# Optimization experiments

Hardware: AMD Instinct MI355X
Metric: run time of the kernel (lower is better)

Reference implementation:

```python
import jax, jax.numpy as jnp
import numpy as np

D_MODEL = 512
T_MAX = 200.0


def setup_inputs() -> dict:
    key = jax.random.key(0)
    k1, k2 = jax.random.split(key)
    B, L = 8, 2048
    event_type = jax.random.randint(k1, (B, L), 0, 2, dtype=jnp.int64 if jax.config.jax_enable_x64 else jnp.int32)
    event_time = jax.random.uniform(k2, (B, L), dtype=jnp.float32) * 200.0
    # learned params (num_types == 1 path)
    length_scale_param = jnp.asarray(1.0, dtype=jnp.float32)   # kernel.length_scale
    gate_params = jnp.asarray([0.1, 0.1], dtype=jnp.float32)   # sigmoid gate (l, s) pre-sigmoid
    return {"event_type": event_type, "event_time": event_time,
            "length_scale_param": length_scale_param, "gate_params": gate_params}


def reference(event_type, event_time, length_scale_param, gate_params):
    B, L = event_time.shape
    # temporal positional encoding: sin on even dims, cos on odd dims
    i = jnp.arange(D_MODEL)
    pos_vec = jnp.power(10000.0, 2.0 * i / D_MODEL).astype(event_time.dtype)
    te = event_time[:, :, None] / pos_vec                      # [B, L, d]
    embedding = jnp.where(i % 2 == 0, jnp.sin(te), jnp.cos(te))

    # pairwise time differences: xt[b,i,j] = t[b,i], xt_bar[b,i,j] = t[b,j]
    t_diff = event_time[:, :, None] - event_time[:, None, :]   # [B, L, L]
    d_abs = jnp.abs(t_diff)                                    # norm = 1

    # squared-exponential kernel (sigma = 1)
    ls = jax.nn.softplus(length_scale_param)
    kern = jnp.exp(-(d_abs ** 2) / (ls ** 2))

    # sigmoid gate: d = |diff / t_max|, gate = 1 + tanh((d - l) / s)
    l = jax.nn.sigmoid(gate_params[0])
    s = jax.nn.sigmoid(gate_params[1])
    gate = 1.0 + jnp.tanh((d_abs / T_MAX - l) / s)

    # causal mask: 1 on lower triangle incl. diagonal, 0 strictly above
    mask = jnp.tril(jnp.ones((L, L), dtype=event_time.dtype))
    scores = kern * gate * mask

    return scores, embedding, t_diff
```

## Files before the change

kernel.cpp:

```cpp
#include <hip/hip_runtime.h>

#define BATCH   8
#define LEN     2048
#define DMODEL  512
#define T_MAX   200.0f

__global__ __launch_bounds__(256) void scores_tdiff_kernel(
    const float* __restrict__ t,
    const float* __restrict__ ls_p,
    const float* __restrict__ gate_p,
    float* __restrict__ scores,
    float* __restrict__ tdiff)
{
    const int row = blockIdx.x;
    const int b   = row >> 11;
    const int i   = row & (LEN - 1);
    const int tid = threadIdx.x;
    const int c0  = tid * 4;
    const int c1  = 1024 + c0;

    const float ti = t[row];

    const float ls      = log1pf(__expf(ls_p[0]));
    const float inv_ls2 = 1.0f / (ls * ls);
    const float l = 1.0f / (1.0f + __expf(-gate_p[0]));
    const float s = 1.0f / (1.0f + __expf(-gate_p[1]));
    const float inv_s2 = 2.0f / s;
    const float invT   = 1.0f / T_MAX;

    const float* trow = t + b * LEN;
    float4 ta = *(const float4*)(trow + c0);
    float4 tb = *(const float4*)(trow + c1);
    float tj[8] = {ta.x, ta.y, ta.z, ta.w, tb.x, tb.y, tb.z, tb.w};
    int   col[8] = {c0, c0 + 1, c0 + 2, c0 + 3, c1, c1 + 1, c1 + 2, c1 + 3};

    float sc[8], td[8];
#pragma unroll
    for (int k = 0; k < 8; ++k) {
        float d  = ti - tj[k];
        float ad = fabsf(d);
        float kern = __expf(-ad * ad * inv_ls2);
        float u2 = (ad * invT - l) * inv_s2;
        float gate = __fdividef(2.0f, 1.0f + __expf(-u2));
        sc[k] = (col[k] <= i) ? kern * gate : 0.0f;
        td[k] = d;
    }

    size_t base = (size_t)row * LEN;
    *(float4*)(scores + base + c0) = make_float4(sc[0], sc[1], sc[2], sc[3]);
    *(float4*)(scores + base + c1) = make_float4(sc[4], sc[5], sc[6], sc[7]);
    *(float4*)(tdiff  + base + c0) = make_float4(td[0], td[1], td[2], td[3]);
    *(float4*)(tdiff  + base + c1) = make_float4(td[4], td[5], td[6], td[7]);
}

__global__ __launch_bounds__(256) void embed_kernel(
    const float* __restrict__ t,
    float* __restrict__ emb)
{
    const int tid = threadIdx.x;
    const int row = blockIdx.x * 2 + (tid >> 7);
    const int d0  = (tid & 127) * 4;

    const float tv = t[row];
    const float c = -9.210340371976184f * (2.0f / (float)DMODEL);

    float e[4];
#pragma unroll
    for (int k = 0; k < 4; k += 2) {
        int dim = d0 + k;
        float inv_pe = __expf(c * (float)dim);
        float inv_po = __expf(c * (float)(dim + 1));
        e[k]     = __sinf(tv * inv_pe);
        e[k + 1] = __cosf(tv * inv_po);
    }
    *(float4*)(emb + (size_t)row * DMODEL + d0) = make_float4(e[0], e[1], e[2], e[3]);
}

extern "C" void kernel_launch(void* const* d_in, const int* in_sizes, int n_in,
                              void* d_out, int out_size, void* d_ws, size_t ws_size,
                              hipStream_t stream) {
    const float* t      = (const float*)d_in[1];
    const float* ls_p   = (const float*)d_in[2];
    const float* gate_p = (const float*)d_in[3];

    float* out = (float*)d_out;
    const size_t n_scores = (size_t)BATCH * LEN * LEN;
    const size_t n_emb    = (size_t)BATCH * LEN * DMODEL;
    float* scores = out;
    float* emb    = out + n_scores;
    float* tdiff  = out + n_scores + n_emb;

    scores_tdiff_kernel<<<BATCH * LEN, 256, 0, stream>>>(t, ls_p, gate_p, scores, tdiff);
    embed_kernel<<<BATCH * LEN / 2, 256, 0, stream>>>(t, emb);
}
```

Baseline: 295.5 us.

## Fuse all outputs into one flat persistent streaming kernel with nontemporal stores

```diff
diff --git a/kernel.cpp b/kernel.cpp
--- a/kernel.cpp
+++ b/kernel.cpp
@@ -5,21 +5,25 @@
 #define DMODEL  512
 #define T_MAX   200.0f
 
-__global__ __launch_bounds__(256) void scores_tdiff_kernel(
+typedef float floatx4 __attribute__((ext_vector_type(4)));
+
+
+#define SC_CHUNKS   8388608u
+#define EMB_CHUNKS  2097152u
+#define TD_CHUNKS   8388608u
+#define EMB_BASE    SC_CHUNKS
+#define TD_BASE     (SC_CHUNKS + EMB_CHUNKS)
+#define NBLOCKS     2048
+#define ITERS       36
+
+__global__ __launch_bounds__(256) void fused_stream_kernel(
     const float* __restrict__ t,
     const float* __restrict__ ls_p,
     const float* __restrict__ gate_p,
-    float* __restrict__ scores,
-    float* __restrict__ tdiff)
+    float* __restrict__ out)
 {
-    const int row = blockIdx.x;
-    const int b   = row >> 11;
-    const int i   = row & (LEN - 1);
-    const int tid = threadIdx.x;
-    const int c0  = tid * 4;
-    const int c1  = 1024 + c0;
-
-    const float ti = t[row];
+    const unsigned tid  = threadIdx.x;
+    const unsigned base = blockIdx.x * (ITERS * 256u);
 
     const float ls      = log1pf(__expf(ls_p[0]));
     const float inv_ls2 = 1.0f / (ls * ls);
@@ -27,53 +31,61 @@
     const float s = 1.0f / (1.0f + __expf(-gate_p[1]));
     const float inv_s2 = 2.0f / s;
     const float invT   = 1.0f / T_MAX;
-
-    const float* trow = t + b * LEN;
-    float4 ta = *(const float4*)(trow + c0);
-    float4 tb = *(const float4*)(trow + c1);
-    float tj[8] = {ta.x, ta.y, ta.z, ta.w, tb.x, tb.y, tb.z, tb.w};
-    int   col[8] = {c0, c0 + 1, c0 + 2, c0 + 3, c1, c1 + 1, c1 + 2, c1 + 3};
-
-    float sc[8], td[8];
-#pragma unroll
-    for (int k = 0; k < 8; ++k) {
-        float d  = ti - tj[k];
-        float ad = fabsf(d);
-        float kern = __expf(-ad * ad * inv_ls2);
-        float u2 = (ad * invT - l) * inv_s2;
-        float gate = __fdividef(2.0f, 1.0f + __expf(-u2));
-        sc[k] = (col[k] <= i) ? kern * gate : 0.0f;
-        td[k] = d;
-    }
-
-    size_t base = (size_t)row * LEN;
-    *(float4*)(scores + base + c0) = make_float4(sc[0], sc[1], sc[2], sc[3]);
-    *(float4*)(scores + base + c1) = make_float4(sc[4], sc[5], sc[6], sc[7]);
-    *(float4*)(tdiff  + base + c0) = make_float4(td[0], td[1], td[2], td[3]);
-    *(float4*)(tdiff  + base + c1) = make_float4(td[4], td[5], td[6], td[7]);
-}
-
-__global__ __launch_bounds__(256) void embed_kernel(
-    const float* __restrict__ t,
-    float* __restrict__ emb)
-{
-    const int tid = threadIdx.x;
-    const int row = blockIdx.x * 2 + (tid >> 7);
-    const int d0  = (tid & 127) * 4;
-
-    const float tv = t[row];
     const float c = -9.210340371976184f * (2.0f / (float)DMODEL);
 
-    float e[4];
+    floatx4* outv = (floatx4*)out;
+
+#pragma unroll 4
+    for (int it = 0; it < ITERS; ++it) {
+        const unsigned g = base + (unsigned)it * 256u + tid;
+
+        if (g < EMB_BASE) {
+            const unsigned e   = g << 2;
+            const unsigned b   = e >> 22;
+            const unsigned rem = e & ((1u << 22) - 1);
+            const unsigned i   = rem >> 11;
+            const unsigned j   = rem & (LEN - 1);
+            const float ti = t[(b << 11) + i];
+            const float4 tj = *(const float4*)(t + (b << 11) + j);
+            const float tjk[4] = {tj.x, tj.y, tj.z, tj.w};
+            floatx4 o;
 #pragma unroll
-    for (int k = 0; k < 4; k += 2) {
-        int dim = d0 + k;
-        float inv_pe = __expf(c * (float)dim);
-        float inv_po = __expf(c * (float)(dim + 1));
-        e[k]     = __sinf(tv * inv_pe);
-        e[k + 1] = __cosf(tv * inv_po);
+            for (int k = 0; k < 4; ++k) {
+                float d  = ti - tjk[k];
+                float ad = fabsf(d);
+                float kern = __expf(-ad * ad * inv_ls2);
+                float u2 = (ad * invT - l) * inv_s2;
+                float gate = __fdividef(2.0f, 1.0f + __expf(-u2));
+                o[k] = (j + (unsigned)k <= i) ? kern * gate : 0.0f;
+            }
+            __builtin_nontemporal_store(o, outv + g);
+        } else if (g < TD_BASE) {
+            const unsigned e   = (g - EMB_BASE) << 2;
+            const unsigned row = e >> 9;
+            const unsigned d0  = e & (DMODEL - 1);
+            const float tv = t[row];
+            floatx4 o;
+            o.x = __sinf(tv * __expf(c * (float)(d0 + 0)));
+            o.y = __cosf(tv * __expf(c * (float)(d0 + 1)));
+            o.z = __sinf(tv * __expf(c * (float)(d0 + 2)));
+            o.w = __cosf(tv * __expf(c * (float)(d0 + 3)));
+            __builtin_nontemporal_store(o, outv + g);
+        } else {
+            const unsigned e   = (g - TD_BASE) << 2;
+            const unsigned b   = e >> 22;
+            const unsigned rem = e & ((1u << 22) - 1);
+            const unsigned i   = rem >> 11;
+            const unsigned j   = rem & (LEN - 1);
+            const float ti = t[(b << 11) + i];
+            const float4 tj = *(const float4*)(t + (b << 11) + j);
+            floatx4 o;
+            o.x = ti - tj.x;
+            o.y = ti - tj.y;
+            o.z = ti - tj.z;
+            o.w = ti - tj.w;
+            __builtin_nontemporal_store(o, outv + g);
+        }
     }
-    *(float4*)(emb + (size_t)row * DMODEL + d0) = make_float4(e[0], e[1], e[2], e[3]);
 }
 
 extern "C" void kernel_launch(void* const* d_in, const int* in_sizes, int n_in,
@@ -83,13 +95,6 @@
     const float* ls_p   = (const float*)d_in[2];
     const float* gate_p = (const float*)d_in[3];
 
-    float* out = (float*)d_out;
-    const size_t n_scores = (size_t)BATCH * LEN * LEN;
-    const size_t n_emb    = (size_t)BATCH * LEN * DMODEL;
-    float* scores = out;
-    float* emb    = out + n_scores;
-    float* tdiff  = out + n_scores + n_emb;
-
-    scores_tdiff_kernel<<<BATCH * LEN, 256, 0, stream>>>(t, ls_p, gate_p, scores, tdiff);
-    embed_kernel<<<BATCH * LEN / 2, 256, 0, stream>>>(t, emb);
+    fused_stream_kernel<<<NBLOCKS, 256, 0, stream>>>(
+        t, ls_p, gate_p, (float*)d_out);
 }
```

Result: slower. 310.3 us (+5.0%).
